# Kernel tuning notes

Hardware: AMD Instinct MI355X
Metric: run time of the kernel (lower is better)

The kernel has to match this reference:

```python
import jax, jax.numpy as jnp
import numpy as np
import math

NUM_HEADS = 16


def setup_inputs() -> dict:
    key = jax.random.key(0)
    k0, k1, k2, k3, k4 = jax.random.split(key, 5)
    B, S, D = 2, 2048, 1024
    scale = 1.0 / math.sqrt(D)
    return {
        "x": jax.random.normal(k0, (B, S, D), dtype=jnp.float32),
        "Wq": jax.random.normal(k1, (D, D), dtype=jnp.float32) * scale,
        "Wk": jax.random.normal(k2, (D, D), dtype=jnp.float32) * scale,
        "Wv": jax.random.normal(k3, (D, D), dtype=jnp.float32) * scale,
        "Wo": jax.random.normal(k4, (D, D), dtype=jnp.float32) * scale,
    }


def reference(x, Wq, Wk, Wv, Wo):
    B, S, D = x.shape
    H = NUM_HEADS
    dk = D // H
    # nn.Linear(bias=False): y = x @ W.T; weights stored [out, in]
    def proj(W):
        return jnp.einsum('bsd,ed->bse', x, W).reshape(B, S, H, dk).transpose(0, 2, 1, 3)
    q = proj(Wq)  # [B, H, S, dk]
    k = proj(Wk)
    v = proj(Wv)
    scores = jnp.einsum('bhqd,bhkd->bhqk', q, k) / jnp.sqrt(jnp.float32(dk))
    causal = jnp.tril(jnp.ones((S, S), dtype=bool))  # True = keep
    scores = jnp.where(causal, scores, -jnp.inf)
    attn = jax.nn.softmax(scores, axis=-1)
    out = jnp.einsum('bhqk,bhkd->bhqd', attn, v)  # [B, H, S, dk]
    out = out.transpose(0, 2, 1, 3).reshape(B, S, D)
    return jnp.einsum('bsd,ed->bse', out, Wo)
```

## Files before the change

### kernel.cpp

```cpp
#include <hip/hip_runtime.h>
#include <hip/hip_bf16.h>

#define S_LEN 2048
#define S_PAD 2112
#define D_DIM 1024
#define N_HEADS 16
#define M_ROWS 4096

typedef __bf16 bf16x8 __attribute__((ext_vector_type(8)));
typedef float f32x4 __attribute__((ext_vector_type(4)));
typedef float f32x16 __attribute__((ext_vector_type(16)));
typedef unsigned short ushortx8 __attribute__((ext_vector_type(8)));
typedef unsigned int uintx4 __attribute__((ext_vector_type(4)));

__device__ __forceinline__ unsigned short f2bf(float f) {
  unsigned int u = __builtin_bit_cast(unsigned int, f);
  u += 0x7fffu + ((u >> 16) & 1u);
  return (unsigned short)(u >> 16);
}

__device__ __forceinline__ unsigned int cvtpk(float lo, float hi) {
  unsigned int r;
  asm("v_cvt_pk_bf16_f32 %0, %1, %2" : "=v"(r) : "v"(lo), "v"(hi));
  return r;
}

__device__ __forceinline__ void pl32swap(unsigned int& a, unsigned int& b) {
  asm("v_permlane32_swap_b32 %0, %1" : "+v"(a), "+v"(b));
}

__device__ __forceinline__ bf16x8 load8(const unsigned short* p) {
  return __builtin_bit_cast(bf16x8, *(const ushortx8*)p);
}

__device__ __forceinline__ void gload16(const unsigned short* g, unsigned short* l) {
  __builtin_amdgcn_global_load_lds((const __attribute__((address_space(1))) void*)g,
                                   (__attribute__((address_space(3))) void*)l,
                                   16, 0, 0);
}

__global__ void cvt5_kernel(const float* __restrict__ s0, const float* __restrict__ s1,
                            const float* __restrict__ s2, const float* __restrict__ s3,
                            const float* __restrict__ s4,
                            unsigned short* __restrict__ d0, unsigned short* __restrict__ d1,
                            unsigned short* __restrict__ d2, unsigned short* __restrict__ d3,
                            unsigned short* __restrict__ d4,
                            int n4x, int n4w) {
  const int y = blockIdx.y;
  const float* s = (y == 0) ? s0 : (y == 1) ? s1 : (y == 2) ? s2 : (y == 3) ? s3 : s4;
  unsigned short* d = (y == 0) ? d0 : (y == 1) ? d1 : (y == 2) ? d2 : (y == 3) ? d3 : d4;
  const int n4 = (y == 0) ? n4x : n4w;
  int i = blockIdx.x * blockDim.x + threadIdx.x;
  if (i < n4) {
    float4 f = ((const float4*)s)[i];
    unsigned int u0 = cvtpk(f.x, f.y), u1 = cvtpk(f.z, f.w);
    unsigned long long packed = (unsigned long long)u0 | ((unsigned long long)u1 << 32);
    ((unsigned long long*)d)[i] = packed;
  }
}

__global__ __launch_bounds__(256) void gemm_bt(
    const unsigned short* __restrict__ A,
    const unsigned short* __restrict__ B0,
    const unsigned short* __restrict__ B1,
    const unsigned short* __restrict__ B2,
    void* __restrict__ C0, void* __restrict__ C1, void* __restrict__ C2,
    int M, int N, int K, int modesel)
{
  __shared__ __align__(16) unsigned short At[128 * 64];
  __shared__ __align__(16) unsigned short Bt[128 * 64];

  const int bid = blockIdx.x + 8 * (blockIdx.y + 32 * blockIdx.z);
  const int k8 = bid & 7, t = bid >> 3;
  const int zz = t >> 5;
  const int u = t & 31;
  const int bxi = (k8 & 1) * 4 + (u & 3);
  const int byi = (k8 >> 1) * 8 + (u >> 2);

  const int z = zz;
  const unsigned short* Bp = (z == 0) ? B0 : (z == 1) ? B1 : B2;
  void* Cp = (z == 0) ? C0 : (z == 1) ? C1 : C2;
  const int mode = (modesel == 0) ? 0 : ((z == 2) ? 2 : 1);
  const float escale = (modesel == 1 && z == 0) ? 0.180336879f : 1.0f;

  const int tid = threadIdx.x;
  const int lane = tid & 63, wave = tid >> 6;
  const int bm = byi * 128, bn = bxi * 128;
  const int wr = wave >> 1, wc = wave & 1;
  const int cl = lane & 15, g = lane >> 4;
  const int ci = lane >> 3, si = lane & 7;
  const int sg = si ^ (ci & 7);

  f32x4 acc[4][4] = {};

  for (int kb = 0; kb < K; kb += 64) {
    __syncthreads();
#pragma unroll
    for (int cc = 0; cc < 4; ++cc) {
      int chunk = wave * 4 + cc;
      int row = chunk * 8 + ci;
      gload16(A  + (size_t)(bm + row) * K + kb + sg * 8, &At[chunk * 512]);
      gload16(Bp + (size_t)(bn + row) * K + kb + sg * 8, &Bt[chunk * 512]);
    }
    __syncthreads();
#pragma unroll
    for (int kc = 0; kc < 2; ++kc) {
      bf16x8 af[4], bfr[4];
#pragma unroll
      for (int mi = 0; mi < 4; ++mi) {
        int row = wr * 64 + mi * 16 + cl;
        int slot = (kc * 4 + g) ^ (row & 7);
        af[mi] = load8(&At[row * 64 + slot * 8]);
      }
#pragma unroll
      for (int ni = 0; ni < 4; ++ni) {
        int row = wc * 64 + ni * 16 + cl;
        int slot = (kc * 4 + g) ^ (row & 7);
        bfr[ni] = load8(&Bt[row * 64 + slot * 8]);
      }
#pragma unroll
      for (int mi = 0; mi < 4; ++mi)
#pragma unroll
        for (int ni = 0; ni < 4; ++ni)
          acc[mi][ni] = __builtin_amdgcn_mfma_f32_16x16x32_bf16(af[mi], bfr[ni], acc[mi][ni], 0, 0, 0);
    }
  }

  const int r0 = g * 4;
#pragma unroll
  for (int mi = 0; mi < 4; ++mi) {
#pragma unroll
    for (int ni = 0; ni < 4; ++ni) {
      int mg = bm + wr * 64 + mi * 16 + r0;
      int ng = bn + wc * 64 + ni * 16 + cl;
#pragma unroll
      for (int r = 0; r < 4; ++r) {
        float v = acc[mi][ni][r] * escale;
        int m = mg + r;
        if (mode == 0) {
          ((float*)Cp)[(size_t)m * N + ng] = v;
        } else {
          int b = m >> 11, s = m & 2047;
          int h = ng >> 6, d = ng & 63;
          unsigned short* o = (unsigned short*)Cp;
          if (mode == 1) o[((size_t)(b * N_HEADS + h) * S_LEN + s) * 64 + d] = f2bf(v);
          else           o[((size_t)(b * N_HEADS + h) * 64 + d) * S_PAD + s] = f2bf(v);
        }
      }
    }
  }
}

__global__ __launch_bounds__(256) void gemm_o64(
    const unsigned short* __restrict__ A,
    const unsigned short* __restrict__ B,
    float* __restrict__ C, int M, int N, int K)
{
  __shared__ __align__(16) unsigned short At[64 * 64];
  __shared__ __align__(16) unsigned short Bt[128 * 64];

  const int bid = blockIdx.x;
  const int k8 = bid & 7, t = bid >> 3;
  const int bxi = t & 7;
  const int byi = k8 * 8 + (t >> 3);

  const int tid = threadIdx.x;
  const int lane = tid & 63, wave = tid >> 6;
  const int bm = byi * 64, bn = bxi * 128;
  const int wr = wave >> 1, wc = wave & 1;
  const int cl = lane & 15, g = lane >> 4;
  const int ci = lane >> 3, si = lane & 7;
  const int sg = si ^ (ci & 7);

  f32x4 acc[2][4] = {};

  for (int kb = 0; kb < K; kb += 64) {
    __syncthreads();
#pragma unroll
    for (int cc = 0; cc < 2; ++cc) {
      int chunk = wave * 2 + cc;
      int row = chunk * 8 + ci;
      gload16(A + (size_t)(bm + row) * K + kb + sg * 8, &At[chunk * 512]);
    }
#pragma unroll
    for (int cc = 0; cc < 4; ++cc) {
      int chunk = wave * 4 + cc;
      int row = chunk * 8 + ci;
      gload16(B + (size_t)(bn + row) * K + kb + sg * 8, &Bt[chunk * 512]);
    }
    __syncthreads();
#pragma unroll
    for (int kc = 0; kc < 2; ++kc) {
      bf16x8 af[2], bfr[4];
#pragma unroll
      for (int mi = 0; mi < 2; ++mi) {
        int row = wr * 32 + mi * 16 + cl;
        int slot = (kc * 4 + g) ^ (row & 7);
        af[mi] = load8(&At[row * 64 + slot * 8]);
      }
#pragma unroll
      for (int ni = 0; ni < 4; ++ni) {
        int row = wc * 64 + ni * 16 + cl;
        int slot = (kc * 4 + g) ^ (row & 7);
        bfr[ni] = load8(&Bt[row * 64 + slot * 8]);
      }
#pragma unroll
      for (int mi = 0; mi < 2; ++mi)
#pragma unroll
        for (int ni = 0; ni < 4; ++ni)
          acc[mi][ni] = __builtin_amdgcn_mfma_f32_16x16x32_bf16(af[mi], bfr[ni], acc[mi][ni], 0, 0, 0);
    }
  }

  const int r0 = g * 4;
#pragma unroll
  for (int mi = 0; mi < 2; ++mi)
#pragma unroll
    for (int ni = 0; ni < 4; ++ni) {
      int mg = bm + wr * 32 + mi * 16 + r0;
      int ng = bn + wc * 64 + ni * 16 + cl;
#pragma unroll
      for (int r = 0; r < 4; ++r)
        C[(size_t)(mg + r) * N + ng] = acc[mi][ni][r];
    }
}

__global__ __launch_bounds__(256) void attn_kernel(
    const unsigned short* __restrict__ Qg,
    const unsigned short* __restrict__ Kg,
    const unsigned short* __restrict__ Vtg,
    unsigned short* __restrict__ Og)
{
  __shared__ __align__(16) unsigned short Kb[2][8192];
  __shared__ __align__(16) unsigned short Vb[2][8192];
  __shared__ __align__(16) unsigned short OB[4][32 * 72];

  const int tid = threadIdx.x;
  const int lane = tid & 63, wave = tid >> 6;
  const int l31 = lane & 31, hi = lane >> 5;

  const int bh = (blockIdx.x & 7) * 4 + ((blockIdx.x >> 3) & 3);
  const int p  = blockIdx.x >> 5;
  const int tA = p, tB = 15 - p;
  const size_t qkb = (size_t)bh * S_LEN;
  const int b = bh >> 4, h = bh & 15;

  int cur = 0;

  auto stageK = [&](int buf, int ch) {
    const unsigned short* base = Kg + (qkb + (size_t)ch * 128) * 64;
#pragma unroll
    for (int ii = 0; ii < 4; ++ii) {
      int i = wave * 4 + ii;
      int ri = i * 8 + (lane >> 3);
      int e = (((lane & 7) ^ (lane >> 3)) << 3);
      gload16(base + (size_t)ri * 64 + e, &Kb[buf][i * 512]);
    }
  };
  auto stageV = [&](int buf, int ch) {
    const unsigned short* base = Vtg + (size_t)bh * 64 * S_PAD + ch * 128;
#pragma unroll
    for (int ii = 0; ii < 4; ++ii) {
      int i = wave * 4 + ii;
      int ri = i * 4 + (lane >> 4);
      int e = (((lane & 15) ^ (ri & 7)) << 3);
      gload16(base + (size_t)ri * S_PAD + e, &Vb[buf][i * 512]);
    }
  };

  const int swz = (l31 & 7) << 3;

  auto kblock = [&](int buf, const bf16x8 (&bq)[4], f32x16 (&o)[2], float& lpart,
                    int j, int jj, bool domask, int qrow) {
    bf16x8 kc[4];
    int krow = j * 32 + l31;
#pragma unroll
    for (int f = 0; f < 4; ++f)
      kc[f] = load8(&Kb[buf][krow * 64 + ((f * 16 + hi * 8) ^ swz)]);
    f32x16 c = {};
    __builtin_amdgcn_s_setprio(1);
#pragma unroll
    for (int f = 0; f < 4; ++f)
      c = __builtin_amdgcn_mfma_f32_32x32x16_bf16(kc[f], bq[f], c, 0, 0, 0);
    __builtin_amdgcn_s_setprio(0);
    if (domask) {
#pragma unroll
      for (int r = 0; r < 16; ++r) {
        int k = jj * 32 + (r & 3) + 8 * (r >> 2) + 4 * hi;
        if (k > qrow) c[r] = -1e30f;
      }
    }
    float s0 = 0.f, s1 = 0.f;
#pragma unroll
    for (int r = 0; r < 16; r += 2) {
      c[r] = __builtin_amdgcn_exp2f(c[r]);         s0 += c[r];
      c[r + 1] = __builtin_amdgcn_exp2f(c[r + 1]); s1 += c[r + 1];
    }
    lpart += s0 + s1;
    bf16x8 pb[2];
#pragma unroll
    for (int kf = 0; kf < 2; ++kf) {
      unsigned int x0 = cvtpk(c[8 * kf + 0], c[8 * kf + 1]);
      unsigned int x1 = cvtpk(c[8 * kf + 2], c[8 * kf + 3]);
      unsigned int y0 = cvtpk(c[8 * kf + 4], c[8 * kf + 5]);
      unsigned int y1 = cvtpk(c[8 * kf + 6], c[8 * kf + 7]);
      pl32swap(x0, y0); pl32swap(x1, y1);
      pb[kf] = __builtin_bit_cast(bf16x8, (uintx4){x0, x1, y0, y1});
    }
    bf16x8 vf[2][2];
#pragma unroll
    for (int kf = 0; kf < 2; ++kf)
#pragma unroll
      for (int dt = 0; dt < 2; ++dt)
        vf[kf][dt] = load8(&Vb[buf][(dt * 32 + l31) * 128 + ((j * 32 + kf * 16 + hi * 8) ^ swz)]);
    __builtin_amdgcn_s_setprio(1);
#pragma unroll
    for (int kf = 0; kf < 2; ++kf)
#pragma unroll
      for (int dt = 0; dt < 2; ++dt)
        o[dt] = __builtin_amdgcn_mfma_f32_32x32x16_bf16(vf[kf][dt], pb[kf], o[dt], 0, 0, 0);
    __builtin_amdgcn_s_setprio(0);
  };

  auto finalize = [&](int qt, f32x16 (&o)[2], float lpart) {
    float lf = lpart + __shfl_xor(lpart, 32, 64);
    float inv = 1.0f / lf;
    unsigned short* W = &OB[wave][0];
#pragma unroll
    for (int dt = 0; dt < 2; ++dt)
#pragma unroll
      for (int rc = 0; rc < 4; ++rc) {
        unsigned int u0 = cvtpk(o[dt][4 * rc] * inv, o[dt][4 * rc + 1] * inv);
        unsigned int u1 = cvtpk(o[dt][4 * rc + 2] * inv, o[dt][4 * rc + 3] * inv);
        unsigned long long pv = (unsigned long long)u0 | ((unsigned long long)u1 << 32);
        *(unsigned long long*)&W[l31 * 72 + dt * 32 + 8 * rc + 4 * hi] = pv;
      }
#pragma unroll
    for (int i = 0; i < 8; ++i) {
      int idx = i * 64 + lane;
      int qr = idx >> 4, c8 = idx & 15;
      unsigned long long v = *(const unsigned long long*)&W[qr * 72 + c8 * 4];
      *(unsigned long long*)&Og[((size_t)(b * S_LEN + qt + wave * 32 + qr)) * D_DIM + h * 64 + c8 * 4] = v;
    }
  };

  auto process_tile = [&](int t, int qt, bool stageNext) {
    bf16x8 bq[4];
#pragma unroll
    for (int f = 0; f < 4; ++f)
      bq[f] = load8(Qg + (qkb + qt + wave * 32 + l31) * 64 + f * 16 + hi * 8);
    f32x16 o[2] = {};
    float lpart = 0.f;

    for (int ch = 0; ch < t; ++ch) {
      stageK(cur ^ 1, ch + 1);
      stageV(cur ^ 1, ch + 1);
#pragma unroll
      for (int j = 0; j < 4; ++j)
        kblock(cur, bq, o, lpart, j, 0, false, 0);
      __syncthreads();
      cur ^= 1;
    }
    if (stageNext) { stageK(cur ^ 1, 0); stageV(cur ^ 1, 0); }
    int qrow = qt + wave * 32 + l31;
    for (int j = 0; j <= wave; ++j)
      kblock(cur, bq, o, lpart, j, 4 * t + j, j == wave, qrow);
    finalize(qt, o, lpart);
    __syncthreads();
    cur ^= 1;
  };

  stageK(0, 0); stageV(0, 0);
  __syncthreads();
  process_tile(tA, tA * 128, true);
  process_tile(tB, tB * 128, false);
}

extern "C" void kernel_launch(void* const* d_in, const int* in_sizes, int n_in,
                              void* d_out, int out_size, void* d_ws, size_t ws_size,
                              hipStream_t stream) {
  const float* x  = (const float*)d_in[0];
  const float* Wq = (const float*)d_in[1];
  const float* Wk = (const float*)d_in[2];
  const float* Wv = (const float*)d_in[3];
  const float* Wo = (const float*)d_in[4];

  const int M = M_ROWS, D = D_DIM;

  unsigned short* ws  = (unsigned short*)d_ws;
  unsigned short* xb  = ws;
  unsigned short* wqb = xb  + (size_t)M * D;
  unsigned short* wkb = wqb + (size_t)D * D;
  unsigned short* wvb = wkb + (size_t)D * D;
  unsigned short* wob = wvb + (size_t)D * D;
  unsigned short* qb  = wob + (size_t)D * D;
  unsigned short* kbf = qb  + (size_t)M * D;
  unsigned short* vtb = kbf + (size_t)M * D;
  unsigned short* aob = vtb + (size_t)32 * 64 * S_PAD;

  {
    dim3 gc(M * D / 4 / 256, 5);
    cvt5_kernel<<<gc, 256, 0, stream>>>(x, Wq, Wk, Wv, Wo,
                                        xb, wqb, wkb, wvb, wob,
                                        M * D / 4, D * D / 4);
  }

  dim3 gq(8, 32, 3);
  gemm_bt<<<gq, 256, 0, stream>>>(xb, wqb, wkb, wvb, qb, kbf, vtb, M, D, D, 1);

  attn_kernel<<<256, 256, 0, stream>>>(qb, kbf, vtb, aob);

  gemm_o64<<<512, 256, 0, stream>>>(aob, wob, (float*)d_out, M, D, D);
}
```

Baseline: 105.9 us.

## Split attention into one query tile per block with 64-key chunks

The attention kernel previously ran 256 blocks, each handling a balanced pair of causal query tiles (t and 15-t) with 128-key double-buffered chunks. It now launches 512 blocks, each handling a single query tile, ordered so the longest tiles are dispatched first. Key chunks shrink to 64, which halves the K/V shared-memory buffers and adjusts the swizzle to match. The aim is higher occupancy and better latency hiding across CUs, at the cost of more barriers per key, re-loading Q in more blocks, and relying on the hardware scheduler rather than explicit pairing for load balance.

```diff
diff --git a/kernel.cpp b/kernel.cpp
--- a/kernel.cpp
+++ b/kernel.cpp
@@ -231,8 +231,8 @@
     const unsigned short* __restrict__ Vtg,
     unsigned short* __restrict__ Og)
 {
-  __shared__ __align__(16) unsigned short Kb[2][8192];
-  __shared__ __align__(16) unsigned short Vb[2][8192];
+  __shared__ __align__(16) unsigned short Kb[2][4096];
+  __shared__ __align__(16) unsigned short Vb[2][4096];
   __shared__ __align__(16) unsigned short OB[4][32 * 72];
 
   const int tid = threadIdx.x;
@@ -240,35 +240,35 @@
   const int l31 = lane & 31, hi = lane >> 5;
 
   const int bh = (blockIdx.x & 7) * 4 + ((blockIdx.x >> 3) & 3);
-  const int p  = blockIdx.x >> 5;
-  const int tA = p, tB = 15 - p;
+  const int t  = 15 - (blockIdx.x >> 5);
+  const int qt = t * 128;
   const size_t qkb = (size_t)bh * S_LEN;
   const int b = bh >> 4, h = bh & 15;
 
   int cur = 0;
 
   auto stageK = [&](int buf, int ch) {
-    const unsigned short* base = Kg + (qkb + (size_t)ch * 128) * 64;
-#pragma unroll
-    for (int ii = 0; ii < 4; ++ii) {
-      int i = wave * 4 + ii;
+    const unsigned short* base = Kg + (qkb + (size_t)ch * 64) * 64;
+#pragma unroll
+    for (int ii = 0; ii < 2; ++ii) {
+      int i = wave * 2 + ii;
       int ri = i * 8 + (lane >> 3);
       int e = (((lane & 7) ^ (lane >> 3)) << 3);
       gload16(base + (size_t)ri * 64 + e, &Kb[buf][i * 512]);
     }
   };
   auto stageV = [&](int buf, int ch) {
-    const unsigned short* base = Vtg + (size_t)bh * 64 * S_PAD + ch * 128;
-#pragma unroll
-    for (int ii = 0; ii < 4; ++ii) {
-      int i = wave * 4 + ii;
-      int ri = i * 4 + (lane >> 4);
-      int e = (((lane & 15) ^ (ri & 7)) << 3);
+    const unsigned short* base = Vtg + (size_t)bh * 64 * S_PAD + ch * 64;
+#pragma unroll
+    for (int ii = 0; ii < 2; ++ii) {
+      int i = wave * 2 + ii;
+      int ri = i * 8 + (lane >> 3);
+      int e = (((lane & 7) ^ (lane >> 3)) << 3);
       gload16(base + (size_t)ri * S_PAD + e, &Vb[buf][i * 512]);
     }
   };
 
-  const int swz = (l31 & 7) << 3;
+  const int sw7 = l31 & 7;
 
   auto kblock = [&](int buf, const bf16x8 (&bq)[4], f32x16 (&o)[2], float& lpart,
                     int j, int jj, bool domask, int qrow) {
@@ -276,7 +276,7 @@
     int krow = j * 32 + l31;
 #pragma unroll
     for (int f = 0; f < 4; ++f)
-      kc[f] = load8(&Kb[buf][krow * 64 + ((f * 16 + hi * 8) ^ swz)]);
+      kc[f] = load8(&Kb[buf][krow * 64 + ((((f << 1) | hi) ^ sw7) << 3)]);
     f32x16 c = {};
     __builtin_amdgcn_s_setprio(1);
 #pragma unroll
@@ -312,7 +312,8 @@
     for (int kf = 0; kf < 2; ++kf)
 #pragma unroll
       for (int dt = 0; dt < 2; ++dt)
-        vf[kf][dt] = load8(&Vb[buf][(dt * 32 + l31) * 128 + ((j * 32 + kf * 16 + hi * 8) ^ swz)]);
+        vf[kf][dt] = load8(&Vb[buf][(dt * 32 + l31) * 64 +
+                                    ((((j << 2) | (kf << 1) | hi) ^ sw7) << 3)]);
     __builtin_amdgcn_s_setprio(1);
 #pragma unroll
     for (int kf = 0; kf < 2; ++kf)
@@ -322,7 +323,7 @@
     __builtin_amdgcn_s_setprio(0);
   };
 
-  auto finalize = [&](int qt, f32x16 (&o)[2], float lpart) {
+  auto finalize = [&](f32x16 (&o)[2], float lpart) {
     float lf = lpart + __shfl_xor(lpart, 32, 64);
     float inv = 1.0f / lf;
     unsigned short* W = &OB[wave][0];
@@ -344,36 +345,38 @@
     }
   };
 
-  auto process_tile = [&](int t, int qt, bool stageNext) {
-    bf16x8 bq[4];
-#pragma unroll
-    for (int f = 0; f < 4; ++f)
-      bq[f] = load8(Qg + (qkb + qt + wave * 32 + l31) * 64 + f * 16 + hi * 8);
-    f32x16 o[2] = {};
-    float lpart = 0.f;
-
-    for (int ch = 0; ch < t; ++ch) {
-      stageK(cur ^ 1, ch + 1);
-      stageV(cur ^ 1, ch + 1);
-#pragma unroll
-      for (int j = 0; j < 4; ++j)
-        kblock(cur, bq, o, lpart, j, 0, false, 0);
-      __syncthreads();
-      cur ^= 1;
-    }
-    if (stageNext) { stageK(cur ^ 1, 0); stageV(cur ^ 1, 0); }
-    int qrow = qt + wave * 32 + l31;
-    for (int j = 0; j <= wave; ++j)
-      kblock(cur, bq, o, lpart, j, 4 * t + j, j == wave, qrow);
-    finalize(qt, o, lpart);
+  bf16x8 bq[4];
+#pragma unroll
+  for (int f = 0; f < 4; ++f)
+    bq[f] = load8(Qg + (qkb + qt + wave * 32 + l31) * 64 + f * 16 + hi * 8);
+
+  f32x16 o[2] = {};
+  float lpart = 0.f;
+  const int qrow = qt + wave * 32 + l31;
+  const int nch = 2 * t + 2;
+
+  stageK(0, 0); stageV(0, 0);
+  __syncthreads();
+
+  for (int ch = 0; ch < nch; ++ch) {
+    if (ch + 1 < nch) { stageK(cur ^ 1, ch + 1); stageV(cur ^ 1, ch + 1); }
+    if (ch < 2 * t) {
+      kblock(cur, bq, o, lpart, 0, 0, false, 0);
+      kblock(cur, bq, o, lpart, 1, 0, false, 0);
+    } else {
+      int tc = ch - 2 * t;
+#pragma unroll
+      for (int j = 0; j < 2; ++j) {
+        int bid32 = 2 * tc + j;
+        if (bid32 <= wave)
+          kblock(cur, bq, o, lpart, j, 4 * t + bid32, bid32 == wave, qrow);
+      }
+    }
     __syncthreads();
     cur ^= 1;
-  };
-
-  stageK(0, 0); stageV(0, 0);
-  __syncthreads();
-  process_tile(tA, tA * 128, true);
-  process_tile(tB, tB * 128, false);
+  }
+
+  finalize(o, lpart);
 }
 
 extern "C" void kernel_launch(void* const* d_in, const int* in_sizes, int n_in,
@@ -408,7 +411,7 @@
   dim3 gq(8, 32, 3);
   gemm_bt<<<gq, 256, 0, stream>>>(xb, wqb, wkb, wvb, qb, kbf, vtb, M, D, D, 1);
 
-  attn_kernel<<<256, 256, 0, stream>>>(qb, kbf, vtb, aob);
+  attn_kernel<<<512, 256, 0, stream>>>(qb, kbf, vtb, aob);
 
   gemm_o64<<<512, 256, 0, stream>>>(aob, wob, (float*)d_out, M, D, D);
 }
```

After: 117.4 us. +10.9%, slower.

## Launch one attention block per query tile instead of paired tiles

Applied to the files above, without the earlier changes.

The attention grid changes from 256 blocks, each processing a causal pair of query tiles (p and 15-p), to 512 blocks that each process a single 128-row query tile, with the longest tiles scheduled first. The LDS staging buffer for the output is also dropped, and each lane writes its 8-byte bf16 chunks directly to global memory. This aims to expose more parallelism across the GPU's CUs and free LDS for occupancy. In exchange it gives up the balanced-pair load scheme, relying on the hardware scheduler to balance uneven causal tiles, and the direct stores are less coalesced.

```diff
diff --git a/kernel.cpp b/kernel.cpp
--- a/kernel.cpp
+++ b/kernel.cpp
@@ -233,15 +233,14 @@
 {
   __shared__ __align__(16) unsigned short Kb[2][8192];
   __shared__ __align__(16) unsigned short Vb[2][8192];
-  __shared__ __align__(16) unsigned short OB[4][32 * 72];
 
   const int tid = threadIdx.x;
   const int lane = tid & 63, wave = tid >> 6;
   const int l31 = lane & 31, hi = lane >> 5;
 
   const int bh = (blockIdx.x & 7) * 4 + ((blockIdx.x >> 3) & 3);
-  const int p  = blockIdx.x >> 5;
-  const int tA = p, tB = 15 - p;
+  const int t  = 15 - (blockIdx.x >> 5);
+  const int qt = t * 128;
   const size_t qkb = (size_t)bh * S_LEN;
   const int b = bh >> 4, h = bh & 15;
 
@@ -322,58 +321,45 @@
     __builtin_amdgcn_s_setprio(0);
   };
 
-  auto finalize = [&](int qt, f32x16 (&o)[2], float lpart) {
+  bf16x8 bq[4];
+#pragma unroll
+  for (int f = 0; f < 4; ++f)
+    bq[f] = load8(Qg + (qkb + qt + wave * 32 + l31) * 64 + f * 16 + hi * 8);
+
+  f32x16 o[2] = {};
+  float lpart = 0.f;
+  const int qrow = qt + wave * 32 + l31;
+
+  stageK(0, 0); stageV(0, 0);
+  __syncthreads();
+
+  for (int ch = 0; ch < t; ++ch) {
+    stageK(cur ^ 1, ch + 1);
+    stageV(cur ^ 1, ch + 1);
+#pragma unroll
+    for (int j = 0; j < 4; ++j)
+      kblock(cur, bq, o, lpart, j, 0, false, 0);
+    __syncthreads();
+    cur ^= 1;
+  }
+  for (int j = 0; j <= wave; ++j)
+    kblock(cur, bq, o, lpart, j, 4 * t + j, j == wave, qrow);
+
+  {
     float lf = lpart + __shfl_xor(lpart, 32, 64);
     float inv = 1.0f / lf;
-    unsigned short* W = &OB[wave][0];
+    unsigned short* base = Og + ((size_t)(b * S_LEN + qt + wave * 32 + l31)) * D_DIM
+                         + h * 64 + 4 * hi;
 #pragma unroll
     for (int dt = 0; dt < 2; ++dt)
 #pragma unroll
       for (int rc = 0; rc < 4; ++rc) {
         unsigned int u0 = cvtpk(o[dt][4 * rc] * inv, o[dt][4 * rc + 1] * inv);
         unsigned int u1 = cvtpk(o[dt][4 * rc + 2] * inv, o[dt][4 * rc + 3] * inv);
-        unsigned long long pv = (unsigned long long)u0 | ((unsigned long long)u1 << 32);
-        *(unsigned long long*)&W[l31 * 72 + dt * 32 + 8 * rc + 4 * hi] = pv;
-      }
-#pragma unroll
-    for (int i = 0; i < 8; ++i) {
-      int idx = i * 64 + lane;
-      int qr = idx >> 4, c8 = idx & 15;
-      unsigned long long v = *(const unsigned long long*)&W[qr * 72 + c8 * 4];
-      *(unsigned long long*)&Og[((size_t)(b * S_LEN + qt + wave * 32 + qr)) * D_DIM + h * 64 + c8 * 4] = v;
-    }
-  };
-
-  auto process_tile = [&](int t, int qt, bool stageNext) {
-    bf16x8 bq[4];
-#pragma unroll
-    for (int f = 0; f < 4; ++f)
-      bq[f] = load8(Qg + (qkb + qt + wave * 32 + l31) * 64 + f * 16 + hi * 8);
-    f32x16 o[2] = {};
-    float lpart = 0.f;
-
-    for (int ch = 0; ch < t; ++ch) {
-      stageK(cur ^ 1, ch + 1);
-      stageV(cur ^ 1, ch + 1);
-#pragma unroll
-      for (int j = 0; j < 4; ++j)
-        kblock(cur, bq, o, lpart, j, 0, false, 0);
-      __syncthreads();
-      cur ^= 1;
-    }
-    if (stageNext) { stageK(cur ^ 1, 0); stageV(cur ^ 1, 0); }
-    int qrow = qt + wave * 32 + l31;
-    for (int j = 0; j <= wave; ++j)
-      kblock(cur, bq, o, lpart, j, 4 * t + j, j == wave, qrow);
-    finalize(qt, o, lpart);
-    __syncthreads();
-    cur ^= 1;
-  };
-
-  stageK(0, 0); stageV(0, 0);
-  __syncthreads();
-  process_tile(tA, tA * 128, true);
-  process_tile(tB, tB * 128, false);
+        *(unsigned long long*)&base[dt * 32 + 8 * rc] =
+            (unsigned long long)u0 | ((unsigned long long)u1 << 32);
+      }
+  }
 }
 
 extern "C" void kernel_launch(void* const* d_in, const int* in_sizes, int n_in,
@@ -408,7 +394,7 @@
   dim3 gq(8, 32, 3);
   gemm_bt<<<gq, 256, 0, stream>>>(xb, wqb, wkb, wvb, qb, kbf, vtb, M, D, D, 1);
 
-  attn_kernel<<<256, 256, 0, stream>>>(qb, kbf, vtb, aob);
+  attn_kernel<<<512, 256, 0, stream>>>(qb, kbf, vtb, aob);
 
   gemm_o64<<<512, 256, 0, stream>>>(aob, wob, (float*)d_out, M, D, D);
 }
```

Measured after the change: 108.2 us. 2.2% more time.
